# Kernel tuning notes

Measured on AMD Instinct MI355X. Metric: run time of the kernel, lower is better.

Reference implementation:

```python
import jax, jax.numpy as jnp
import numpy as np

BSZ, L, D_INNER, D_STATE = 2, 2048, 2048, 8
DT_RANK = D_INNER // 8  # 256


def setup_inputs() -> dict:
    key = jax.random.key(0)
    k0, k1, k2, k3 = jax.random.split(key, 4)
    x = jax.random.normal(k0, (BSZ, L, D_INNER), jnp.float32)
    # x_proj: Linear(d_inner -> dt_rank + 2*d_state), no bias
    W_xproj = jax.random.normal(k1, (DT_RANK + 2 * D_STATE, D_INNER), jnp.float32) * 0.02
    # dt_proj: Linear(dt_rank -> d_inner), uniform(-dt_rank^-0.5, +)
    std = DT_RANK ** -0.5
    W_dt = jax.random.uniform(k2, (D_INNER, DT_RANK), jnp.float32, -std, std)
    # dt bias init: inverse-softplus of dt ~ LogUniform(1e-3, 1e-1)
    dt = jnp.exp(jax.random.uniform(k3, (D_INNER,), jnp.float32)
                 * (jnp.log(0.1) - jnp.log(0.001)) + jnp.log(0.001))
    dt = jnp.clip(dt, 1e-4)
    b_dt = dt + jnp.log(-jnp.expm1(-dt))
    # A = repeat(arange(1, N+1), 'n -> d n'); A_log = log(A)
    A_log = jnp.log(jnp.broadcast_to(
        jnp.arange(1, D_STATE + 1, dtype=jnp.float32), (D_INNER, D_STATE)))
    D_param = jnp.ones((D_INNER,), jnp.float32)
    return {"x": x, "W_xproj": W_xproj, "W_dt": W_dt, "b_dt": b_dt,
            "A_log": A_log, "D_param": D_param}


def reference(x, W_xproj, W_dt, b_dt, A_log, D_param):
    # x: (B, L, D)
    d_state = A_log.shape[1]
    dt_rank = W_dt.shape[1]
    x_dbl = jnp.einsum('bld,kd->blk', x, W_xproj)          # (B,L,dt_rank+2N)
    dt_r = x_dbl[..., :dt_rank]
    B_ssm = x_dbl[..., dt_rank:dt_rank + d_state]          # (B,L,N)
    C_ssm = x_dbl[..., dt_rank + d_state:]                 # (B,L,N)
    delta = jax.nn.softplus(jnp.einsum('blr,dr->bld', dt_r, W_dt) + b_dt)  # (B,L,D) > 0
    A = -jnp.exp(A_log)                                     # (D,N) < 0
    # Discretization: dA = exp(delta*A), dBu = delta*B*u
    dA = jnp.exp(delta[..., None] * A)                      # (B,L,D,N)
    dBu = (delta * x)[..., None] * B_ssm[:, :, None, :]     # (B,L,D,N)

    # Linear recurrence h_t = dA_t * h_{t-1} + dBu_t via associative scan over L
    def combine(c1, c2):
        a1, b1 = c1
        a2, b2 = c2
        return a1 * a2, a2 * b1 + b2

    _, h = jax.lax.associative_scan(combine, (dA, dBu), axis=1)  # (B,L,D,N)
    y = jnp.einsum('bldn,bln->bld', h, C_ssm) + x * D_param
    return y
```

## Files before the change

### kernel.cpp

```cpp
#include <hip/hip_runtime.h>
#include <math.h>

#define BSZ    2
#define LSEQ   2048
#define DI     2048
#define DSTATE 8
#define DTRANK 256
#define KXP    (DTRANK + 2 * DSTATE)
#define NPAD   288
#define NC     64
#define CL     (LSEQ / NC)
#define KSPLIT 4

#define NWXP (288u * 2048u)
#define NWX  (272u * 2048u)
#define NWDT (2048u * 256u)

typedef __attribute__((ext_vector_type(8))) short bf16x8;
typedef __attribute__((ext_vector_type(4))) float f32x4;

static __device__ __forceinline__ unsigned short f2bf(float f) {
    unsigned u = __float_as_uint(f);
    u += 0x7fff + ((u >> 16) & 1);
    return (unsigned short)(u >> 16);
}

static __device__ __forceinline__ float softplus_fast(float z) {
    const float e = __expf(-fabsf(z));
    return fmaxf(z, 0.0f) + __logf(1.0f + e);
}

__global__ __launch_bounds__(256) void convert_w(const float* __restrict__ Wx,
                                                 const float* __restrict__ Wdt,
                                                 unsigned short* __restrict__ Wxb,
                                                 unsigned short* __restrict__ Wdtb) {
    const unsigned tid = blockIdx.x * 256 + threadIdx.x;
    const unsigned i4 = tid * 4;
    float4 v;
    unsigned short* dst;
    unsigned j;
    if (i4 < NWXP) {
        j = i4;
        v = (j < NWX) ? *(const float4*)&Wx[j] : make_float4(0.f, 0.f, 0.f, 0.f);
        dst = Wxb;
    } else {
        j = i4 - NWXP;
        if (j >= NWDT) return;
        v = *(const float4*)&Wdt[j];
        dst = Wdtb;
    }
    ushort4 o;
    o.x = f2bf(v.x); o.y = f2bf(v.y); o.z = f2bf(v.z); o.w = f2bf(v.w);
    *(ushort4*)&dst[j] = o;
}

__global__ __launch_bounds__(256, 1) void gemm1_mfma(const float* __restrict__ x,
                                                     const unsigned short* __restrict__ Wxb,
                                                     float* __restrict__ part) {
    const int mt   = blockIdx.x;
    const int ks   = blockIdx.y;
    const int wave = threadIdx.x >> 6;
    const int lane = threadIdx.x & 63;
    const int quad = lane >> 4;
    const int r    = lane & 15;
    const int kq   = quad * 8;
    const int mbase = mt * 64 + wave * 16;
    const size_t arow = (size_t)(mbase + r) * DI;
    const size_t brow = (size_t)r * DI;

    f32x4 acc[18];
#pragma unroll
    for (int n = 0; n < 18; n++) acc[n] = (f32x4)(0.0f);

    const int kbeg = ks * (DI / KSPLIT);
#pragma unroll 2
    for (int k0 = kbeg; k0 < kbeg + DI / KSPLIT; k0 += 32) {
        const float4 u0 = *(const float4*)&x[arow + k0 + kq];
        const float4 u1 = *(const float4*)&x[arow + k0 + kq + 4];
        bf16x8 a;
        a[0] = (short)f2bf(u0.x); a[1] = (short)f2bf(u0.y);
        a[2] = (short)f2bf(u0.z); a[3] = (short)f2bf(u0.w);
        a[4] = (short)f2bf(u1.x); a[5] = (short)f2bf(u1.y);
        a[6] = (short)f2bf(u1.z); a[7] = (short)f2bf(u1.w);
#pragma unroll
        for (int nf = 0; nf < 18; nf++) {
            const bf16x8 b = *(const bf16x8*)&Wxb[brow + nf * (16 * DI) + k0 + kq];
            acc[nf] = __builtin_amdgcn_mfma_f32_16x16x32_bf16(a, b, acc[nf], 0, 0, 0);
        }
    }

    float* p = part + (size_t)ks * 4096 * NPAD;
    const int row0 = mbase + quad * 4;
#pragma unroll
    for (int nf = 0; nf < 18; nf++) {
        const int col = nf * 16 + r;
#pragma unroll
        for (int i = 0; i < 4; i++)
            p[(size_t)(row0 + i) * NPAD + col] = acc[nf][i];
    }
}

__global__ __launch_bounds__(256) void reduce1(const float* __restrict__ part,
                                               float* __restrict__ xdbl,
                                               unsigned short* __restrict__ dtr) {
    const int tid = blockIdx.x * 256 + threadIdx.x;
    const int row = tid / 72;
    const int c4  = (tid - row * 72) * 4;
    float4 s = make_float4(0.f, 0.f, 0.f, 0.f);
#pragma unroll
    for (int ks = 0; ks < KSPLIT; ks++) {
        const float4 v = *(const float4*)&part[(size_t)ks * 4096 * NPAD + (size_t)row * NPAD + c4];
        s.x += v.x; s.y += v.y; s.z += v.z; s.w += v.w;
    }
    if (c4 < KXP) *(float4*)&xdbl[(size_t)row * KXP + c4] = s;
    if (c4 < DTRANK) {
        ushort4 o;
        o.x = f2bf(s.x); o.y = f2bf(s.y); o.z = f2bf(s.z); o.w = f2bf(s.w);
        *(ushort4*)&dtr[(size_t)row * DTRANK + c4] = o;
    }
}

#define G2RS 40
__global__ __launch_bounds__(256, 2) void gemm2_mfma(const unsigned short* __restrict__ dtr,
                                                     const unsigned short* __restrict__ Wdtb,
                                                     const float* __restrict__ bdt,
                                                     float* __restrict__ delta) {
    __shared__ __align__(16) unsigned short As[128 * G2RS];
    __shared__ __align__(16) unsigned short Bs[128 * G2RS];
    const int nt   = blockIdx.x;
    const int mt   = blockIdx.y;
    const int t    = threadIdx.x;
    const int wave = t >> 6;
    const int lane = t & 63;
    const int quad = lane >> 4;
    const int r    = lane & 15;
    const int m0 = mt * 128, n0 = nt * 128;
    const int mw = (wave >> 1) * 64, nw = (wave & 1) * 64;

    const int srow = t >> 1;
    const int sc   = (t & 1) * 16;

    f32x4 acc[4][4];
#pragma unroll
    for (int f = 0; f < 4; f++)
#pragma unroll
        for (int g = 0; g < 4; g++) acc[f][g] = (f32x4)(0.0f);

    for (int k0 = 0; k0 < DTRANK; k0 += 32) {
        const bf16x8 a0 = *(const bf16x8*)&dtr[(size_t)(m0 + srow) * DTRANK + k0 + sc];
        const bf16x8 a1 = *(const bf16x8*)&dtr[(size_t)(m0 + srow) * DTRANK + k0 + sc + 8];
        const bf16x8 b0 = *(const bf16x8*)&Wdtb[(size_t)(n0 + srow) * DTRANK + k0 + sc];
        const bf16x8 b1 = *(const bf16x8*)&Wdtb[(size_t)(n0 + srow) * DTRANK + k0 + sc + 8];
        __syncthreads();
        *(bf16x8*)&As[srow * G2RS + sc]     = a0;
        *(bf16x8*)&As[srow * G2RS + sc + 8] = a1;
        *(bf16x8*)&Bs[srow * G2RS + sc]     = b0;
        *(bf16x8*)&Bs[srow * G2RS + sc + 8] = b1;
        __syncthreads();

        bf16x8 a[4], b[4];
#pragma unroll
        for (int f = 0; f < 4; f++)
            a[f] = *(const bf16x8*)&As[(mw + f * 16 + r) * G2RS + quad * 8];
#pragma unroll
        for (int g = 0; g < 4; g++)
            b[g] = *(const bf16x8*)&Bs[(nw + g * 16 + r) * G2RS + quad * 8];
#pragma unroll
        for (int f = 0; f < 4; f++)
#pragma unroll
            for (int g = 0; g < 4; g++)
                acc[f][g] = __builtin_amdgcn_mfma_f32_16x16x32_bf16(a[f], b[g], acc[f][g], 0, 0, 0);
    }

#pragma unroll
    for (int f = 0; f < 4; f++) {
        const int row0 = m0 + mw + f * 16 + quad * 4;
#pragma unroll
        for (int g = 0; g < 4; g++) {
            const int col = n0 + nw + g * 16 + r;
            const float bv = bdt[col];
#pragma unroll
            for (int i = 0; i < 4; i++)
                delta[(size_t)(row0 + i) * DI + col] = softplus_fast(acc[f][g][i] + bv);
        }
    }
}

__global__ __launch_bounds__(256) void scan_pass1(const float* __restrict__ x,
                                                  const float* __restrict__ delta,
                                                  const float* __restrict__ xdbl,
                                                  const float* __restrict__ Alog,
                                                  float* __restrict__ Pb,
                                                  float* __restrict__ Hb) {
    __shared__ __align__(16) float Ls[CL * 8];
    const int bi   = blockIdx.x;
    const int b    = bi >> 9;
    const int c    = (bi >> 3) & 63;
    const int dblk = bi & 7;
    const int d    = dblk * 256 + threadIdx.x;
    const int l0   = c * CL;
    const size_t row0 = (size_t)b * LSEQ + l0;

    if (threadIdx.x < CL * 2) {
        const int l = threadIdx.x >> 1, part = (threadIdx.x & 1) * 4;
        const float4 v = *(const float4*)&xdbl[(row0 + l) * KXP + DTRANK + part];
        *(float4*)&Ls[l * 8 + part] = v;
    }

    float A[8], h[8], P[8];
#pragma unroll
    for (int n = 0; n < 8; n++) {
        A[n] = -__expf(Alog[d * 8 + n]);
        h[n] = 0.f;
        P[n] = 1.f;
    }
    __syncthreads();

#pragma unroll 4
    for (int l = 0; l < CL; l++) {
        const size_t row = row0 + l;
        const float dl = delta[row * DI + d];
        const float xv = x[row * DI + d];
        const float du = dl * xv;
#pragma unroll
        for (int n = 0; n < 8; n++) {
            const float dA = __expf(dl * A[n]);
            h[n] = dA * h[n] + du * Ls[l * 8 + n];
            P[n] *= dA;
        }
    }
    const size_t base = ((size_t)(b * NC + c) * DI + d) * 8;
    *(float4*)&Pb[base]     = make_float4(P[0], P[1], P[2], P[3]);
    *(float4*)&Pb[base + 4] = make_float4(P[4], P[5], P[6], P[7]);
    *(float4*)&Hb[base]     = make_float4(h[0], h[1], h[2], h[3]);
    *(float4*)&Hb[base + 4] = make_float4(h[4], h[5], h[6], h[7]);
}

__global__ __launch_bounds__(256) void scan_pass2(const float* __restrict__ Pb,
                                                  const float* __restrict__ Hb,
                                                  float* __restrict__ h0) {
    const int t   = blockIdx.x * 256 + threadIdx.x;
    const int b   = t >> 14;
    const int rem = t & 16383;
    float h = 0.f;
#pragma unroll 4
    for (int c = 0; c < NC; c++) {
        const size_t base = (size_t)(b * NC + c) * (DI * 8) + rem;
        h0[base] = h;
        h = Pb[base] * h + Hb[base];
    }
}

__global__ __launch_bounds__(256) void scan_pass3(const float* __restrict__ x,
                                                  const float* __restrict__ delta,
                                                  const float* __restrict__ xdbl,
                                                  const float* __restrict__ Alog,
                                                  const float* __restrict__ Dp,
                                                  const float* __restrict__ h0,
                                                  float* __restrict__ y) {
    __shared__ __align__(16) float Ls[CL * 16];
    const int bi   = blockIdx.x;
    const int b    = bi >> 9;
    const int c    = (bi >> 3) & 63;
    const int dblk = bi & 7;
    const int d    = dblk * 256 + threadIdx.x;
    const int l0   = c * CL;
    const size_t row0 = (size_t)b * LSEQ + l0;

    if (threadIdx.x < CL * 4) {
        const int l = threadIdx.x >> 2, part = (threadIdx.x & 3) * 4;
        const float4 v = *(const float4*)&xdbl[(row0 + l) * KXP + DTRANK + part];
        *(float4*)&Ls[l * 16 + part] = v;
    }

    float A[8], h[8];
    const size_t hbase = ((size_t)(b * NC + c) * DI + d) * 8;
    const float4 h0a = *(const float4*)&h0[hbase];
    const float4 h0b = *(const float4*)&h0[hbase + 4];
    h[0] = h0a.x; h[1] = h0a.y; h[2] = h0a.z; h[3] = h0a.w;
    h[4] = h0b.x; h[5] = h0b.y; h[6] = h0b.z; h[7] = h0b.w;
#pragma unroll
    for (int n = 0; n < 8; n++) A[n] = -__expf(Alog[d * 8 + n]);
    const float Dpar = Dp[d];
    __syncthreads();

#pragma unroll 4
    for (int l = 0; l < CL; l++) {
        const size_t row = row0 + l;
        const float dl = delta[row * DI + d];
        const float xv = x[row * DI + d];
        const float du = dl * xv;
        float yv = 0.f;
#pragma unroll
        for (int n = 0; n < 8; n++) {
            const float dA = __expf(dl * A[n]);
            h[n] = dA * h[n] + du * Ls[l * 16 + n];
            yv += h[n] * Ls[l * 16 + 8 + n];
        }
        yv += xv * Dpar;
        y[row * DI + d] = yv;
    }
}

extern "C" void kernel_launch(void* const* d_in, const int* in_sizes, int n_in,
                              void* d_out, int out_size, void* d_ws, size_t ws_size,
                              hipStream_t stream) {
    const float* x    = (const float*)d_in[0];
    const float* Wx   = (const float*)d_in[1];
    const float* Wdt  = (const float*)d_in[2];
    const float* bdt  = (const float*)d_in[3];
    const float* Alog = (const float*)d_in[4];
    const float* Dp   = (const float*)d_in[5];
    float* y = (float*)d_out;

    float* ws    = (float*)d_ws;
    float* part  = ws;
    float* delta = ws;
    float* xdbl  = ws + 8388608;
    float* Pb    = xdbl + 1114112;
    float* Hb    = Pb + 2097152;
    float* h0    = Hb + 2097152;
    unsigned short* Wxb  = (unsigned short*)(h0 + 2097152);
    unsigned short* Wdtb = Wxb + (size_t)NWXP;
    unsigned short* dtr  = Wdtb + (size_t)NWDT;

    dim3 blk(256);
    hipLaunchKernelGGL(convert_w, dim3((NWXP + NWDT) / 4 / 256), blk, 0, stream,
                       Wx, Wdt, Wxb, Wdtb);
    hipLaunchKernelGGL(gemm1_mfma, dim3(64, KSPLIT), blk, 0, stream, x, Wxb, part);
    hipLaunchKernelGGL(reduce1, dim3(4096 * 72 / 256), blk, 0, stream, part, xdbl, dtr);
    hipLaunchKernelGGL(gemm2_mfma, dim3(16, 32), blk, 0, stream, dtr, Wdtb, bdt, delta);
    hipLaunchKernelGGL(scan_pass1, dim3(BSZ * NC * 8), blk, 0, stream, x, delta, xdbl, Alog, Pb, Hb);
    hipLaunchKernelGGL(scan_pass2, dim3(128), blk, 0, stream, Pb, Hb, h0);
    hipLaunchKernelGGL(scan_pass3, dim3(BSZ * NC * 8), blk, 0, stream, x, delta, xdbl, Alog, Dp, h0, y);
}
```

Measured before the change: 200.0 us.

## Split gemm1 across more blocks and store split-K partials in bf16

```diff
diff --git a/kernel.cpp b/kernel.cpp
--- a/kernel.cpp
+++ b/kernel.cpp
@@ -10,7 +10,7 @@
 #define NPAD   288
 #define NC     64
 #define CL     (LSEQ / NC)
-#define KSPLIT 4
+#define KSPLIT 8
 
 #define NWXP (288u * 2048u)
 #define NWX  (272u * 2048u)
@@ -23,6 +23,9 @@
     unsigned u = __float_as_uint(f);
     u += 0x7fff + ((u >> 16) & 1);
     return (unsigned short)(u >> 16);
+}
+static __device__ __forceinline__ float bf2f(unsigned short s) {
+    return __uint_as_float((unsigned)s << 16);
 }
 
 static __device__ __forceinline__ float softplus_fast(float z) {
@@ -54,9 +57,9 @@
     *(ushort4*)&dst[j] = o;
 }
 
-__global__ __launch_bounds__(256, 1) void gemm1_mfma(const float* __restrict__ x,
-                                                     const unsigned short* __restrict__ Wxb,
-                                                     float* __restrict__ part) {
+__global__ __launch_bounds__(256) void gemm1_mfma(const float* __restrict__ x,
+                                                  const unsigned short* __restrict__ Wxb,
+                                                  unsigned short* __restrict__ partb) {
     const int mt   = blockIdx.x;
     const int ks   = blockIdx.y;
     const int wave = threadIdx.x >> 6;
@@ -64,13 +67,16 @@
     const int quad = lane >> 4;
     const int r    = lane & 15;
     const int kq   = quad * 8;
-    const int mbase = mt * 64 + wave * 16;
+    const int rh   = wave >> 1;
+    const int nh   = wave & 1;
+    const int mbase  = mt * 32 + rh * 16;
+    const int nfrag0 = nh * 9;
     const size_t arow = (size_t)(mbase + r) * DI;
     const size_t brow = (size_t)r * DI;
 
-    f32x4 acc[18];
-#pragma unroll
-    for (int n = 0; n < 18; n++) acc[n] = (f32x4)(0.0f);
+    f32x4 acc[9];
+#pragma unroll
+    for (int n = 0; n < 9; n++) acc[n] = (f32x4)(0.0f);
 
     const int kbeg = ks * (DI / KSPLIT);
 #pragma unroll 2
@@ -83,24 +89,24 @@
         a[4] = (short)f2bf(u1.x); a[5] = (short)f2bf(u1.y);
         a[6] = (short)f2bf(u1.z); a[7] = (short)f2bf(u1.w);
 #pragma unroll
-        for (int nf = 0; nf < 18; nf++) {
-            const bf16x8 b = *(const bf16x8*)&Wxb[brow + nf * (16 * DI) + k0 + kq];
+        for (int nf = 0; nf < 9; nf++) {
+            const bf16x8 b = *(const bf16x8*)&Wxb[brow + (size_t)(nfrag0 + nf) * (16 * DI) + k0 + kq];
             acc[nf] = __builtin_amdgcn_mfma_f32_16x16x32_bf16(a, b, acc[nf], 0, 0, 0);
         }
     }
 
-    float* p = part + (size_t)ks * 4096 * NPAD;
+    unsigned short* p = partb + (size_t)ks * 4096 * NPAD;
     const int row0 = mbase + quad * 4;
 #pragma unroll
-    for (int nf = 0; nf < 18; nf++) {
-        const int col = nf * 16 + r;
+    for (int nf = 0; nf < 9; nf++) {
+        const int col = (nfrag0 + nf) * 16 + r;
 #pragma unroll
         for (int i = 0; i < 4; i++)
-            p[(size_t)(row0 + i) * NPAD + col] = acc[nf][i];
-    }
-}
-
-__global__ __launch_bounds__(256) void reduce1(const float* __restrict__ part,
+            p[(size_t)(row0 + i) * NPAD + col] = f2bf(acc[nf][i]);
+    }
+}
+
+__global__ __launch_bounds__(256) void reduce1(const unsigned short* __restrict__ partb,
                                                float* __restrict__ xdbl,
                                                unsigned short* __restrict__ dtr) {
     const int tid = blockIdx.x * 256 + threadIdx.x;
@@ -109,8 +115,8 @@
     float4 s = make_float4(0.f, 0.f, 0.f, 0.f);
 #pragma unroll
     for (int ks = 0; ks < KSPLIT; ks++) {
-        const float4 v = *(const float4*)&part[(size_t)ks * 4096 * NPAD + (size_t)row * NPAD + c4];
-        s.x += v.x; s.y += v.y; s.z += v.z; s.w += v.w;
+        const ushort4 v = *(const ushort4*)&partb[(size_t)ks * 4096 * NPAD + (size_t)row * NPAD + c4];
+        s.x += bf2f(v.x); s.y += bf2f(v.y); s.z += bf2f(v.z); s.w += bf2f(v.w);
     }
     if (c4 < KXP) *(float4*)&xdbl[(size_t)row * KXP + c4] = s;
     if (c4 < DTRANK) {
@@ -314,7 +320,7 @@
     float* y = (float*)d_out;
 
     float* ws    = (float*)d_ws;
-    float* part  = ws;
+    unsigned short* partb = (unsigned short*)ws;
     float* delta = ws;
     float* xdbl  = ws + 8388608;
     float* Pb    = xdbl + 1114112;
@@ -327,8 +333,8 @@
     dim3 blk(256);
     hipLaunchKernelGGL(convert_w, dim3((NWXP + NWDT) / 4 / 256), blk, 0, stream,
                        Wx, Wdt, Wxb, Wdtb);
-    hipLaunchKernelGGL(gemm1_mfma, dim3(64, KSPLIT), blk, 0, stream, x, Wxb, part);
-    hipLaunchKernelGGL(reduce1, dim3(4096 * 72 / 256), blk, 0, stream, part, xdbl, dtr);
+    hipLaunchKernelGGL(gemm1_mfma, dim3(128, KSPLIT), blk, 0, stream, x, Wxb, partb);
+    hipLaunchKernelGGL(reduce1, dim3(4096 * 72 / 256), blk, 0, stream, partb, xdbl, dtr);
     hipLaunchKernelGGL(gemm2_mfma, dim3(16, 32), blk, 0, stream, dtr, Wdtb, bdt, delta);
     hipLaunchKernelGGL(scan_pass1, dim3(BSZ * NC * 8), blk, 0, stream, x, delta, xdbl, Alog, Pb, Hb);
     hipLaunchKernelGGL(scan_pass2, dim3(128), blk, 0, stream, Pb, Hb, h0);
```

New measurement: 205.7 us. 1.03x slower.
